# Kernel tuning notes

Hardware: AMD Instinct MI355X
Metric: run time of the kernel (lower is better)

Reference implementation:

```python
import jax, jax.numpy as jnp
import numpy as np

N_DRUGS = 4096
W_DIM = 512
N_SUB = 10
N_EDGES = 131072


def setup_inputs() -> dict:
    key = jax.random.key(0)
    k1, k2, k3, k4 = jax.random.split(key, 4)
    z_drug = jax.random.normal(k1, (N_DRUGS, W_DIM), dtype=jnp.float32)
    # glorot-ish init for weights
    global_weight = jax.random.normal(k2, (W_DIM, W_DIM), dtype=jnp.float32) * (2.0 / (2 * W_DIM)) ** 0.5
    local_diag = jax.random.normal(k3, (N_SUB, W_DIM), dtype=jnp.float32) * (2.0 / (W_DIM + 1)) ** 0.5
    batch_edges = jax.random.randint(k4, (2, N_EDGES), 0, N_DRUGS, dtype=jnp.int64)
    return {
        "z_drug": z_drug,
        "global_weight": global_weight,
        "local_diag": local_diag,
        "batch_edges": batch_edges,
        "edge_sub_type_idx": 2,
    }


def reference(z_drug, global_weight, local_diag, batch_edges, edge_sub_type_idx):
    # edge_type == 'drug_drug': z1 = z2 = z_drug
    row_embed = z_drug[batch_edges[0]]            # [B, D]
    col_embed = z_drug[batch_edges[1]]            # [B, D]
    d = local_diag[edge_sub_type_idx]             # [D] diagonal of local weight matrix
    # row @ diag(d) @ W @ diag(d) == ((row * d) @ W) * d
    p = ((row_embed * d) @ global_weight) * d     # [B, D]
    # diagonal(p @ col^T) == rowwise dot product
    score = jnp.sum(p * col_embed, axis=-1)       # [B]
    return jax.nn.sigmoid(score)
```

## Files before the change

kernel.cpp:

```cpp
#include <hip/hip_runtime.h>
#include <cstdint>

#define ND 4096
#define D  512

typedef __bf16 bf16x8 __attribute__((ext_vector_type(8)));
typedef float floatx4 __attribute__((ext_vector_type(4)));
typedef unsigned short ushort8 __attribute__((ext_vector_type(8)));

__device__ __forceinline__ float bf2f(unsigned short b) {
    return __uint_as_float(((unsigned int)b) << 16);
}
__device__ __forceinline__ unsigned short f2bf(float f) {
    unsigned int u = __float_as_uint(f);
    u += 0x7fffu + ((u >> 16) & 1u);
    return (unsigned short)(u >> 16);
}
__device__ __forceinline__ float lo16(unsigned int u) { return __uint_as_float(u << 16); }
__device__ __forceinline__ float hi16(unsigned int u) { return __uint_as_float(u & 0xffff0000u); }

__device__ __forceinline__ void gll16(const void* g, void* l) {
    __builtin_amdgcn_global_load_lds((const __attribute__((address_space(1))) unsigned int*)g,
                                     (__attribute__((address_space(3))) unsigned int*)l,
                                     16, 0, 0);
}

union U8B8 { ushort8 u; bf16x8 b; };

__device__ __forceinline__ int2 detect_flags(const unsigned short* z, const int* ed) {
    int lane = threadIdx.x & 63;
    unsigned short u = z[lane];
    int e = (u >> 7) & 0xFF;
    unsigned long long b0 = __ballot(e >= 96 && e <= 160);
    unsigned long long b1 = __ballot(ed[2 * lane + 1] == 0);
    int2 f;
    f.x = (__popcll(b0) >= 56) ? 1 : 0;
    f.y = (__popcll(b1) >= 56) ? 1 : 0;
    return f;
}

__global__ __launch_bounds__(256) void make_mt(const void* __restrict__ Wv,
                                               const void* __restrict__ ldv,
                                               const int* __restrict__ sub,
                                               unsigned short* __restrict__ Mt,
                                               const unsigned short* __restrict__ zdet,
                                               const int* __restrict__ eddet) {
    __shared__ float xp[64][65];
    int2 f = detect_flags(zdet, eddet);
    int bf = f.x;
    int su = sub[0];
    if ((unsigned)su > 9u) su = 2;
    int k0 = (blockIdx.x & 7) * 64, n0 = (blockIdx.x >> 3) * 64;
    int j = threadIdx.x & 63, w = threadIdx.x >> 6;
#pragma unroll
    for (int r = 0; r < 16; r++) {
        int k = k0 + w * 16 + r;
        float v = bf ? bf2f(((const unsigned short*)Wv)[k * D + n0 + j])
                     : ((const float*)Wv)[k * D + n0 + j];
        xp[w * 16 + r][j] = v;
    }
    __syncthreads();
    int k = k0 + j;
    float dk = bf ? bf2f(((const unsigned short*)ldv)[su * D + k])
                  : ((const float*)ldv)[su * D + k];
#pragma unroll
    for (int r = 0; r < 16; r++) {
        int n = n0 + w * 16 + r;
        float dn = bf ? bf2f(((const unsigned short*)ldv)[su * D + n])
                      : ((const float*)ldv)[su * D + n];
        Mt[n * D + k] = f2bf(xp[j][w * 16 + r] * dk * dn);
    }
}

template <bool BF>
__device__ void gemm_body(const void* __restrict__ z, const unsigned short* __restrict__ Mt,
                          unsigned short* __restrict__ Y) {
    __shared__ __bf16 As[8 * 512];
    __shared__ __bf16 Bs[8 * 512];
    int tid = threadIdx.x;
    int w = tid >> 6, lane = tid & 63;
    int rl = lane & 15, quad = lane >> 4;
    int tm = (blockIdx.x >> 3) * 64, tn = (blockIdx.x & 7) * 64;
    int wm = (w >> 1) * 32, wn = (w & 1) * 32;

    floatx4 acc[2][2] = {};
    for (int kk = 0; kk < D; kk += 64) {
        __syncthreads();
#pragma unroll
        for (int t = 0; t < 2; t++) {
            int kb = w * 2 + t;
            gll16(Mt + (tn + lane) * D + kk + kb * 8, Bs + kb * 512);
            if constexpr (BF) {
                gll16((const __bf16*)z + (tm + lane) * D + kk + kb * 8, As + kb * 512);
            } else {
                const float* zf = (const float*)z + (tm + lane) * D + kk + kb * 8;
                float4 f0 = *(const float4*)zf;
                float4 f1 = *(const float4*)(zf + 4);
                U8B8 cv;
                cv.u[0] = f2bf(f0.x); cv.u[1] = f2bf(f0.y); cv.u[2] = f2bf(f0.z); cv.u[3] = f2bf(f0.w);
                cv.u[4] = f2bf(f1.x); cv.u[5] = f2bf(f1.y); cv.u[6] = f2bf(f1.z); cv.u[7] = f2bf(f1.w);
                *(bf16x8*)(As + kb * 512 + lane * 8) = cv.b;
            }
        }
        __syncthreads();
#pragma unroll
        for (int kc = 0; kc < 64; kc += 32) {
            int kb0 = kc >> 3;
            bf16x8 a0 = *(const bf16x8*)(As + (kb0 + quad) * 512 + (wm + rl) * 8);
            bf16x8 a1 = *(const bf16x8*)(As + (kb0 + quad) * 512 + (wm + 16 + rl) * 8);
            bf16x8 b0 = *(const bf16x8*)(Bs + (kb0 + quad) * 512 + (wn + rl) * 8);
            bf16x8 b1 = *(const bf16x8*)(Bs + (kb0 + quad) * 512 + (wn + 16 + rl) * 8);
            acc[0][0] = __builtin_amdgcn_mfma_f32_16x16x32_bf16(a0, b0, acc[0][0], 0, 0, 0);
            acc[0][1] = __builtin_amdgcn_mfma_f32_16x16x32_bf16(a0, b1, acc[0][1], 0, 0, 0);
            acc[1][0] = __builtin_amdgcn_mfma_f32_16x16x32_bf16(a1, b0, acc[1][0], 0, 0, 0);
            acc[1][1] = __builtin_amdgcn_mfma_f32_16x16x32_bf16(a1, b1, acc[1][1], 0, 0, 0);
        }
    }
#pragma unroll
    for (int j = 0; j < 2; j++) {
        int col = tn + wn + j * 16 + rl;
#pragma unroll
        for (int i = 0; i < 2; i++) {
            int rbase = tm + wm + i * 16 + quad * 4;
#pragma unroll
            for (int r = 0; r < 4; r++)
                Y[(rbase + r) * D + col] = f2bf(acc[i][j][r]);
        }
    }
}

__global__ __launch_bounds__(256) void gemm_kernel(const void* __restrict__ z,
                                                   const unsigned short* __restrict__ Mt,
                                                   unsigned short* __restrict__ Y,
                                                   const int* __restrict__ eddet) {
    int2 f = detect_flags((const unsigned short*)z, eddet);
    if (f.x) gemm_body<true>(z, Mt, Y);
    else     gemm_body<false>(z, Mt, Y);
}

template <bool BF, bool I64>
__device__ void edge_slice_body(const unsigned short* __restrict__ Y,
                                const void* __restrict__ z,
                                const int* __restrict__ ed,
                                float* __restrict__ partial, int E) {
    int slice = blockIdx.x & 7;
    int egrp  = blockIdx.x >> 3;
    int lane = threadIdx.x & 63;
    int w = threadIdx.x >> 6;
    int sub8 = lane >> 3;
    int l = lane & 7;
    int col = slice * 64 + l * 8;

#pragma unroll
    for (int i = 0; i < 8; i++) {
        int e = egrp * 256 + i * 32 + w * 8 + sub8;
        if (e >= E) break;
        int r, c;
        if constexpr (I64) { r = ed[2 * e]; c = ed[2 * (E + e)]; }
        else               { r = ed[e];     c = ed[E + e]; }
        r &= ND - 1; c &= ND - 1;

        uint4 yu = *(const uint4*)(Y + r * D + col);
        float s;
        if constexpr (BF) {
            uint4 zu = *(const uint4*)((const unsigned short*)z + c * D + col);
            s  = lo16(yu.x) * lo16(zu.x) + hi16(yu.x) * hi16(zu.x);
            s += lo16(yu.y) * lo16(zu.y) + hi16(yu.y) * hi16(zu.y);
            s += lo16(yu.z) * lo16(zu.z) + hi16(yu.z) * hi16(zu.z);
            s += lo16(yu.w) * lo16(zu.w) + hi16(yu.w) * hi16(zu.w);
        } else {
            const float* zf = (const float*)z + c * D + col;
            float4 f0 = *(const float4*)zf;
            float4 f1 = *(const float4*)(zf + 4);
            s  = lo16(yu.x) * f0.x + hi16(yu.x) * f0.y;
            s += lo16(yu.y) * f0.z + hi16(yu.y) * f0.w;
            s += lo16(yu.z) * f1.x + hi16(yu.z) * f1.y;
            s += lo16(yu.w) * f1.z + hi16(yu.w) * f1.w;
        }
        s += __shfl_xor(s, 1, 64);
        s += __shfl_xor(s, 2, 64);
        s += __shfl_xor(s, 4, 64);
        if (l == 0)
            partial[slice * E + e] = s;
    }
}

__global__ __launch_bounds__(256) void edge_slice(const unsigned short* __restrict__ Y,
                                                  const void* __restrict__ z,
                                                  const int* __restrict__ ed,
                                                  float* __restrict__ partial, int E) {
    int2 f = detect_flags((const unsigned short*)z, ed);
    if (f.x) { if (f.y) edge_slice_body<true, true >(Y, z, ed, partial, E);
               else     edge_slice_body<true, false>(Y, z, ed, partial, E); }
    else     { if (f.y) edge_slice_body<false, true >(Y, z, ed, partial, E);
               else     edge_slice_body<false, false>(Y, z, ed, partial, E); }
}

__global__ __launch_bounds__(256) void finish_kernel(const float* __restrict__ partial,
                                                     const unsigned short* __restrict__ zdet,
                                                     const int* __restrict__ eddet,
                                                     void* __restrict__ out, int E) {
    int2 f = detect_flags(zdet, eddet);
    int e = blockIdx.x * 256 + threadIdx.x;
    if (e >= E) return;
    float t = 0.f;
#pragma unroll
    for (int s = 0; s < 8; s++)
        t += partial[s * E + e];
    if (!(t > -1e30f && t < 1e30f)) t = 0.0f;
    float sig = 1.0f / (1.0f + __expf(-t));
    if (f.x) ((unsigned short*)out)[e] = f2bf(sig);
    else     ((float*)out)[e] = sig;
}

extern "C" void kernel_launch(void* const* d_in, const int* in_sizes, int n_in,
                              void* d_out, int out_size, void* d_ws, size_t ws_size,
                              hipStream_t stream) {
    const void* z     = d_in[0];
    const void* W     = d_in[1];
    const void* ldiag = d_in[2];
    const int* edges  = (const int*)d_in[3];
    const int* sub    = (const int*)d_in[4];
    int E = out_size;

    char* ws = (char*)d_ws;
    unsigned short* Y  = (unsigned short*)ws;
    unsigned short* Mt = (unsigned short*)(ws + 4194304);
    float* partial     = (float*)(ws + 4194304 + 524288);

    make_mt<<<64, 256, 0, stream>>>(W, ldiag, sub, Mt, (const unsigned short*)z, edges);
    gemm_kernel<<<512, 256, 0, stream>>>(z, Mt, Y, edges);
    int sblocks = ((E + 255) / 256) * 8;
    edge_slice<<<sblocks, 256, 0, stream>>>(Y, z, edges, partial, E);
    finish_kernel<<<(E + 255) / 256, 256, 0, stream>>>(partial, (const unsigned short*)z,
                                                       edges, d_out, E);
}
```

Before: 109.7 us.

## Pre-convert z to bf16, double-buffer GEMM LDS, remap tiles per XCD, batch edge gathers

A prep kernel now also converts fp32 z to bf16 into workspace, so the GEMM can stage both operands with direct global-to-LDS loads. The GEMM double-buffers its LDS tiles to overlap the next load with the current MFMAs, and it remaps block indices so each XCD covers a contiguous group of row tiles. The edge kernel hoists all eight index loads and gathers ahead of the reductions to expose more memory-level parallelism. In exchange it uses an extra 4 MB workspace buffer, an extra read and write pass over z, and more registers per thread.

```diff
diff --git a/kernel.cpp b/kernel.cpp
--- a/kernel.cpp
+++ b/kernel.cpp
@@ -39,15 +39,36 @@
     return f;
 }
 
-__global__ __launch_bounds__(256) void make_mt(const void* __restrict__ Wv,
-                                               const void* __restrict__ ldv,
-                                               const int* __restrict__ sub,
-                                               unsigned short* __restrict__ Mt,
-                                               const unsigned short* __restrict__ zdet,
-                                               const int* __restrict__ eddet) {
+__global__ __launch_bounds__(256) void prep_kernel(const void* __restrict__ Wv,
+                                                   const void* __restrict__ ldv,
+                                                   const int* __restrict__ sub,
+                                                   unsigned short* __restrict__ Mt,
+                                                   unsigned short* __restrict__ zb,
+                                                   const void* __restrict__ z,
+                                                   const int* __restrict__ ed) {
     __shared__ float xp[64][65];
-    int2 f = detect_flags(zdet, eddet);
+    int2 f = detect_flags((const unsigned short*)z, ed);
     int bf = f.x;
+
+    if (blockIdx.x >= 64) {
+        if (bf) return;
+        int idx = (int)(blockIdx.x - 64) * 256 + threadIdx.x;
+        const float* zf = (const float*)z;
+#pragma unroll
+        for (int it = 0; it < 4; it++) {
+            int base = (it * 65536 + idx) * 8;
+            float4 f0 = *(const float4*)(zf + base);
+            float4 f1 = *(const float4*)(zf + base + 4);
+            union { ushort8 u; uint4 v; } cv;
+            cv.u[0] = f2bf(f0.x); cv.u[1] = f2bf(f0.y);
+            cv.u[2] = f2bf(f0.z); cv.u[3] = f2bf(f0.w);
+            cv.u[4] = f2bf(f1.x); cv.u[5] = f2bf(f1.y);
+            cv.u[6] = f2bf(f1.z); cv.u[7] = f2bf(f1.w);
+            *(uint4*)(zb + base) = cv.v;
+        }
+        return;
+    }
+
     int su = sub[0];
     if ((unsigned)su > 9u) su = 2;
     int k0 = (blockIdx.x & 7) * 64, n0 = (blockIdx.x >> 3) * 64;
@@ -72,50 +93,64 @@
     }
 }
 
-template <bool BF>
-__device__ void gemm_body(const void* __restrict__ z, const unsigned short* __restrict__ Mt,
-                          unsigned short* __restrict__ Y) {
-    __shared__ __bf16 As[8 * 512];
-    __shared__ __bf16 Bs[8 * 512];
+__global__ __launch_bounds__(256) void gemm_kernel(const void* __restrict__ z,
+                                                   const unsigned short* __restrict__ zb,
+                                                   const unsigned short* __restrict__ Mt,
+                                                   unsigned short* __restrict__ Y,
+                                                   const int* __restrict__ ed) {
+    __shared__ __bf16 As[2][8 * 512];
+    __shared__ __bf16 Bs[2][8 * 512];
+    int2 f = detect_flags((const unsigned short*)z, ed);
+    const unsigned short* A = f.x ? (const unsigned short*)z : zb;
+
     int tid = threadIdx.x;
     int w = tid >> 6, lane = tid & 63;
     int rl = lane & 15, quad = lane >> 4;
-    int tm = (blockIdx.x >> 3) * 64, tn = (blockIdx.x & 7) * 64;
+    int bx = blockIdx.x;
+    int xcd = bx & 7, idx = bx >> 3;
+    int tm = (xcd * 8 + (idx & 7)) * 64;
+    int tn = (idx >> 3) * 64;
     int wm = (w >> 1) * 32, wn = (w & 1) * 32;
 
+    const unsigned short* Ap = A + (tm + lane) * D;
+    const unsigned short* Bp = Mt + (tn + lane) * D;
+
     floatx4 acc[2][2] = {};
-    for (int kk = 0; kk < D; kk += 64) {
-        __syncthreads();
+
+    auto stage = [&](int buf, int kk) {
 #pragma unroll
         for (int t = 0; t < 2; t++) {
             int kb = w * 2 + t;
-            gll16(Mt + (tn + lane) * D + kk + kb * 8, Bs + kb * 512);
-            if constexpr (BF) {
-                gll16((const __bf16*)z + (tm + lane) * D + kk + kb * 8, As + kb * 512);
-            } else {
-                const float* zf = (const float*)z + (tm + lane) * D + kk + kb * 8;
-                float4 f0 = *(const float4*)zf;
-                float4 f1 = *(const float4*)(zf + 4);
-                U8B8 cv;
-                cv.u[0] = f2bf(f0.x); cv.u[1] = f2bf(f0.y); cv.u[2] = f2bf(f0.z); cv.u[3] = f2bf(f0.w);
-                cv.u[4] = f2bf(f1.x); cv.u[5] = f2bf(f1.y); cv.u[6] = f2bf(f1.z); cv.u[7] = f2bf(f1.w);
-                *(bf16x8*)(As + kb * 512 + lane * 8) = cv.b;
-            }
-        }
-        __syncthreads();
+            gll16(Bp + kk + kb * 8, &Bs[buf][kb * 512]);
+            gll16(Ap + kk + kb * 8, &As[buf][kb * 512]);
+        }
+    };
+    auto compute = [&](int buf) {
 #pragma unroll
         for (int kc = 0; kc < 64; kc += 32) {
             int kb0 = kc >> 3;
-            bf16x8 a0 = *(const bf16x8*)(As + (kb0 + quad) * 512 + (wm + rl) * 8);
-            bf16x8 a1 = *(const bf16x8*)(As + (kb0 + quad) * 512 + (wm + 16 + rl) * 8);
-            bf16x8 b0 = *(const bf16x8*)(Bs + (kb0 + quad) * 512 + (wn + rl) * 8);
-            bf16x8 b1 = *(const bf16x8*)(Bs + (kb0 + quad) * 512 + (wn + 16 + rl) * 8);
+            bf16x8 a0 = *(const bf16x8*)(&As[buf][(kb0 + quad) * 512 + (wm + rl) * 8]);
+            bf16x8 a1 = *(const bf16x8*)(&As[buf][(kb0 + quad) * 512 + (wm + 16 + rl) * 8]);
+            bf16x8 b0 = *(const bf16x8*)(&Bs[buf][(kb0 + quad) * 512 + (wn + rl) * 8]);
+            bf16x8 b1 = *(const bf16x8*)(&Bs[buf][(kb0 + quad) * 512 + (wn + 16 + rl) * 8]);
             acc[0][0] = __builtin_amdgcn_mfma_f32_16x16x32_bf16(a0, b0, acc[0][0], 0, 0, 0);
             acc[0][1] = __builtin_amdgcn_mfma_f32_16x16x32_bf16(a0, b1, acc[0][1], 0, 0, 0);
             acc[1][0] = __builtin_amdgcn_mfma_f32_16x16x32_bf16(a1, b0, acc[1][0], 0, 0, 0);
             acc[1][1] = __builtin_amdgcn_mfma_f32_16x16x32_bf16(a1, b1, acc[1][1], 0, 0, 0);
         }
-    }
+    };
+
+    stage(0, 0);
+    __syncthreads();
+#pragma unroll
+    for (int kt = 1; kt < 8; kt++) {
+        int cur = (kt - 1) & 1;
+        stage(cur ^ 1, kt * 64);
+        compute(cur);
+        __syncthreads();
+    }
+    compute(1);
+
 #pragma unroll
     for (int j = 0; j < 2; j++) {
         int col = tn + wn + j * 16 + rl;
@@ -127,15 +162,6 @@
                 Y[(rbase + r) * D + col] = f2bf(acc[i][j][r]);
         }
     }
-}
-
-__global__ __launch_bounds__(256) void gemm_kernel(const void* __restrict__ z,
-                                                   const unsigned short* __restrict__ Mt,
-                                                   unsigned short* __restrict__ Y,
-                                                   const int* __restrict__ eddet) {
-    int2 f = detect_flags((const unsigned short*)z, eddet);
-    if (f.x) gemm_body<true>(z, Mt, Y);
-    else     gemm_body<false>(z, Mt, Y);
 }
 
 template <bool BF, bool I64>
@@ -150,38 +176,76 @@
     int sub8 = lane >> 3;
     int l = lane & 7;
     int col = slice * 64 + l * 8;
-
-#pragma unroll
-    for (int i = 0; i < 8; i++) {
-        int e = egrp * 256 + i * 32 + w * 8 + sub8;
-        if (e >= E) break;
-        int r, c;
-        if constexpr (I64) { r = ed[2 * e]; c = ed[2 * (E + e)]; }
-        else               { r = ed[e];     c = ed[E + e]; }
-        r &= ND - 1; c &= ND - 1;
-
-        uint4 yu = *(const uint4*)(Y + r * D + col);
-        float s;
-        if constexpr (BF) {
-            uint4 zu = *(const uint4*)((const unsigned short*)z + c * D + col);
-            s  = lo16(yu.x) * lo16(zu.x) + hi16(yu.x) * hi16(zu.x);
-            s += lo16(yu.y) * lo16(zu.y) + hi16(yu.y) * hi16(zu.y);
-            s += lo16(yu.z) * lo16(zu.z) + hi16(yu.z) * hi16(zu.z);
-            s += lo16(yu.w) * lo16(zu.w) + hi16(yu.w) * hi16(zu.w);
-        } else {
-            const float* zf = (const float*)z + c * D + col;
-            float4 f0 = *(const float4*)zf;
-            float4 f1 = *(const float4*)(zf + 4);
-            s  = lo16(yu.x) * f0.x + hi16(yu.x) * f0.y;
-            s += lo16(yu.y) * f0.z + hi16(yu.y) * f0.w;
-            s += lo16(yu.z) * f1.x + hi16(yu.z) * f1.y;
-            s += lo16(yu.w) * f1.z + hi16(yu.w) * f1.w;
-        }
-        s += __shfl_xor(s, 1, 64);
-        s += __shfl_xor(s, 2, 64);
-        s += __shfl_xor(s, 4, 64);
-        if (l == 0)
-            partial[slice * E + e] = s;
+    int e0 = egrp * 256 + w * 8 + sub8;
+
+    if (egrp * 256 + 255 < E) {
+        int r[8], c[8];
+#pragma unroll
+        for (int i = 0; i < 8; i++) {
+            int e = e0 + i * 32;
+            if constexpr (I64) { r[i] = ed[2 * e] & (ND - 1); c[i] = ed[2 * (E + e)] & (ND - 1); }
+            else               { r[i] = ed[e] & (ND - 1);     c[i] = ed[E + e] & (ND - 1); }
+        }
+        float s[8];
+#pragma unroll
+        for (int i = 0; i < 8; i++) {
+            uint4 yu = *(const uint4*)(Y + r[i] * D + col);
+            if constexpr (BF) {
+                uint4 zu = *(const uint4*)((const unsigned short*)z + c[i] * D + col);
+                s[i]  = lo16(yu.x) * lo16(zu.x) + hi16(yu.x) * hi16(zu.x);
+                s[i] += lo16(yu.y) * lo16(zu.y) + hi16(yu.y) * hi16(zu.y);
+                s[i] += lo16(yu.z) * lo16(zu.z) + hi16(yu.z) * hi16(zu.z);
+                s[i] += lo16(yu.w) * lo16(zu.w) + hi16(yu.w) * hi16(zu.w);
+            } else {
+                const float* zf = (const float*)z + c[i] * D + col;
+                float4 f0 = *(const float4*)zf;
+                float4 f1 = *(const float4*)(zf + 4);
+                s[i]  = lo16(yu.x) * f0.x + hi16(yu.x) * f0.y;
+                s[i] += lo16(yu.y) * f0.z + hi16(yu.y) * f0.w;
+                s[i] += lo16(yu.z) * f1.x + hi16(yu.z) * f1.y;
+                s[i] += lo16(yu.w) * f1.z + hi16(yu.w) * f1.w;
+            }
+        }
+#pragma unroll
+        for (int i = 0; i < 8; i++) {
+            s[i] += __shfl_xor(s[i], 1, 64);
+            s[i] += __shfl_xor(s[i], 2, 64);
+            s[i] += __shfl_xor(s[i], 4, 64);
+            if (l == 0)
+                partial[slice * E + e0 + i * 32] = s[i];
+        }
+    } else {
+#pragma unroll
+        for (int i = 0; i < 8; i++) {
+            int e = e0 + i * 32;
+            if (e >= E) continue;
+            int r, c;
+            if constexpr (I64) { r = ed[2 * e]; c = ed[2 * (E + e)]; }
+            else               { r = ed[e];     c = ed[E + e]; }
+            r &= ND - 1; c &= ND - 1;
+            uint4 yu = *(const uint4*)(Y + r * D + col);
+            float s;
+            if constexpr (BF) {
+                uint4 zu = *(const uint4*)((const unsigned short*)z + c * D + col);
+                s  = lo16(yu.x) * lo16(zu.x) + hi16(yu.x) * hi16(zu.x);
+                s += lo16(yu.y) * lo16(zu.y) + hi16(yu.y) * hi16(zu.y);
+                s += lo16(yu.z) * lo16(zu.z) + hi16(yu.z) * hi16(zu.z);
+                s += lo16(yu.w) * lo16(zu.w) + hi16(yu.w) * hi16(zu.w);
+            } else {
+                const float* zf = (const float*)z + c * D + col;
+                float4 f0 = *(const float4*)zf;
+                float4 f1 = *(const float4*)(zf + 4);
+                s  = lo16(yu.x) * f0.x + hi16(yu.x) * f0.y;
+                s += lo16(yu.y) * f0.z + hi16(yu.y) * f0.w;
+                s += lo16(yu.z) * f1.x + hi16(yu.z) * f1.y;
+                s += lo16(yu.w) * f1.z + hi16(yu.w) * f1.w;
+            }
+            s += __shfl_xor(s, 1, 64);
+            s += __shfl_xor(s, 2, 64);
+            s += __shfl_xor(s, 4, 64);
+            if (l == 0)
+                partial[slice * E + e] = s;
+        }
     }
 }
 
@@ -227,9 +291,10 @@
     unsigned short* Y  = (unsigned short*)ws;
     unsigned short* Mt = (unsigned short*)(ws + 4194304);
     float* partial     = (float*)(ws + 4194304 + 524288);
-
-    make_mt<<<64, 256, 0, stream>>>(W, ldiag, sub, Mt, (const unsigned short*)z, edges);
-    gemm_kernel<<<512, 256, 0, stream>>>(z, Mt, Y, edges);
+    unsigned short* zb = (unsigned short*)(ws + 4194304 + 524288 + 4194304);
+
+    prep_kernel<<<320, 256, 0, stream>>>(W, ldiag, sub, Mt, zb, z, edges);
+    gemm_kernel<<<512, 256, 0, stream>>>(z, zb, Mt, Y, edges);
     int sblocks = ((E + 255) / 256) * 8;
     edge_slice<<<sblocks, 256, 0, stream>>>(Y, z, edges, partial, E);
     finish_kernel<<<(E + 255) / 256, 256, 0, stream>>>(partial, (const unsigned short*)z,
```

New measurement: 107.2 us. -2.3%, faster.
